# Kernel optimization log

Hardware: AMD Instinct MI355X
Metric: run time of the kernel (lower is better)

## Reference

```python
import jax, jax.numpy as jnp
import numpy as np

jax.config.update("jax_enable_x64", True)

B, S = 256, 256
TINY = float(np.finfo(np.float64).tiny)  # torch.finfo().tiny for double


def _matrix_tree_logZ(scores, mask):
    """scores: [B,S,S] float64, mask: [B,S] bool (col 0 is False).
    Returns sum over batch of log partition function (Matrix-Tree theorem)."""
    lens = mask.sum(-1)  # token counts per sentence (excludes root col)
    mask_r = mask.at[:, 0].set(True)  # index_fill(1, 0, 1)
    pair = mask_r[:, :, None] & mask_r[:, None, :]  # [B,S,S]
    s = jnp.where(pair, scores, -jnp.inf)
    m = jnp.max(s.reshape(s.shape[0], -1), axis=-1)  # [B] per-batch max for stability
    A = jnp.maximum(jnp.exp(s - m[:, None, None]), TINY)  # clamp like torch
    idx = jnp.arange(S)
    D = jnp.zeros_like(A).at[:, idx, idx].set(A.sum(-1))  # degree matrix
    eye = jnp.eye(S, dtype=A.dtype)
    # masked_scatter_: rows with mask_r True take (D - A) rows, else identity
    L = jnp.where(mask_r[:, :, None], D - A, eye)
    logZ = jnp.linalg.slogdet(L[:, 1:, 1:])[1] + m * lens
    return logZ.sum()


def setup_inputs() -> dict:
    key = jax.random.key(0)
    k1, k2 = jax.random.split(key)
    scores = jax.random.normal(k1, (B, S, S), dtype=jnp.float32)
    lens = jax.random.randint(k2, (B,), S // 2, S)  # sentence lengths
    pos = jnp.arange(S)
    # col 0 (pseudo root) False, padding beyond length False
    mask = (pos[None, :] >= 1) & (pos[None, :] < lens[:, None])
    return {"scores": scores, "mask": mask}


def reference(scores, mask):
    # mbr=True path: marginals = d logZ / d scores (computed in double like torch)
    s64 = scores.astype(jnp.float64)
    probs = jax.grad(_matrix_tree_logZ)(s64, mask)
    return probs.astype(jnp.float32)
```

## Files before the change

kernel.cpp:

```cpp
#include <hip/hip_runtime.h>
#include <math.h>


#define S 256
#define BB 256

__device__ __forceinline__ int rowmap(int lr, int kb) {
    int rt = lr >> 6;
    int rb = rt + (rt >= kb ? 1 : 0);
    return rb * 64 + (lr & 63);
}

__global__ __launch_bounds__(256) void k_max(const float* __restrict__ sc,
                                             float* __restrict__ partial) {
    int b = blockIdx.y, rg = blockIdx.x;
    const float4* p4 = (const float4*)(sc + (size_t)b * S * S + rg * 8192);
    int tid = threadIdx.x;
    float4 v[8];
    #pragma unroll
    for (int it = 0; it < 8; ++it) v[it] = p4[tid + 256 * it];
    float m = -1e30f;
    #pragma unroll
    for (int it = 0; it < 8; ++it)
        m = fmaxf(m, fmaxf(fmaxf(v[it].x, v[it].y), fmaxf(v[it].z, v[it].w)));
    for (int off = 32; off > 0; off >>= 1) m = fmaxf(m, __shfl_down(m, off));
    __shared__ float sm[4];
    if ((tid & 63) == 0) sm[tid >> 6] = m;
    __syncthreads();
    if (tid == 0) partial[b * 8 + rg] = fmaxf(fmaxf(sm[0], sm[1]), fmaxf(sm[2], sm[3]));
}

__global__ void k_n(const unsigned char* __restrict__ mk, const float* __restrict__ partial,
                    double* __restrict__ mb, int* __restrict__ nb) {
    int b = blockIdx.x, j = threadIdx.x;
    __shared__ int shc[4];

    const unsigned int* mw = (const unsigned int*)mk;
    unsigned int w0 = mw[0], w1 = mw[1];
    int mode = (w0 != 0u) ? 0 : ((w1 != 0u) ? 1 : 2);

    int c;
    if (mode == 0)      c = (mk[(size_t)b * S + j] != 0);
    else if (mode == 1) c = (((const int*)mk)[(size_t)b * S + j] != 0);
    else                c = (((const long long*)mk)[(size_t)b * S + j] != 0LL);

    int lane = j & 63, wid = j >> 6;
    int cs = c;
    for (int off = 32; off > 0; off >>= 1) cs += __shfl_down(cs, off);
    if (lane == 0) shc[wid] = cs;
    __syncthreads();
    if (j == 0) {
        nb[b] = shc[0] + shc[1] + shc[2] + shc[3];
        float mm = partial[b * 8];
        #pragma unroll
        for (int q = 1; q < 8; ++q) mm = fmaxf(mm, partial[b * 8 + q]);
        mb[b] = (double)mm;
    }
}

__global__ __launch_bounds__(256) void k_build(const float* __restrict__ sc,
                                               const double* __restrict__ mb,
                                               const int* __restrict__ nb,
                                               double* __restrict__ Mg) {
    int b = blockIdx.y;
    int wid = threadIdx.x >> 6, lane = threadIdx.x & 63;
    int p = blockIdx.x * 4 + wid;
    int n = nb[b];
    double m = mb[b];
    __shared__ double se[4][260];
    double* Mrow = Mg + ((size_t)b * S + p) * S;
    bool act = (p < n);
    double ssum = 0.0;
    #pragma unroll
    for (int c4 = 0; c4 < 4; ++c4) {
        int j = lane + 64 * c4;
        double ev = 0.0;
        if (act && j <= n)
            ev = (double)expf((float)((double)sc[((size_t)b * S + (p + 1)) * S + j] - m));
        se[wid][j] = ev;
        ssum += ev;
    }
    for (int off = 32; off > 0; off >>= 1) ssum += __shfl_down(ssum, off);
    ssum = __shfl(ssum, 0);
    __syncthreads();
    #pragma unroll
    for (int c4 = 0; c4 < 4; ++c4) {
        int j = lane + 64 * c4;
        double v;
        if (act && j < n) v = ((j == p) ? ssum : 0.0) - se[wid][j + 1];
        else              v = (j == p) ? 1.0 : 0.0;
        Mrow[j] = v;
    }
}

__global__ __launch_bounds__(512) void k_step(double* __restrict__ Mg, int kb) {
    int b = blockIdx.x;
    double* M = Mg + (size_t)b * S * S;
    int tid = threadIdx.x;
    __shared__ double H[64 * 256];
    __shared__ double SCR[3104];

    int i = tid >> 3, g = tid & 7, c0 = g << 3;
    double c[8];
    {
        const double* src = M + (size_t)(kb * 64 + i) * S + kb * 64 + c0;
        #pragma unroll
        for (int m2 = 0; m2 < 4; ++m2) {
            double2 t = *(const double2*)(src + 2 * m2);
            c[2 * m2] = t.x; c[2 * m2 + 1] = t.y;
        }
    }
    double* rbuf = SCR;
    double* cbuf = SCR + 128;
    if (i == 0) {
        #pragma unroll
        for (int u = 0; u < 8; ++u) rbuf[c0 + u] = c[u];
    }
    if (g == 0) cbuf[i] = c[0];
    for (int k = 0; k < 64; ++k) {
        int par = k & 1;
        __syncthreads();
        double pv = rbuf[par * 64 + k];
        double f  = cbuf[par * 64 + i];
        double rk[8];
        #pragma unroll
        for (int m2 = 0; m2 < 4; ++m2) {
            double2 t = *(const double2*)&rbuf[par * 64 + c0 + 2 * m2];
            rk[2 * m2] = t.x; rk[2 * m2 + 1] = t.y;
        }
        double pivinv = 1.0 / pv;
        int kg = k >> 3, ks = k & 7;
        if (i == k) {
            #pragma unroll
            for (int u = 0; u < 8; ++u)
                c[u] = ((g == kg) && (u == ks)) ? pivinv : c[u] * pivinv;
        } else {
            double gm = f * pivinv;
            #pragma unroll
            for (int u = 0; u < 8; ++u)
                c[u] = ((g == kg) && (u == ks)) ? (-gm) : fma(-gm, rk[u], c[u]);
        }
        int k1 = k + 1;
        if (k1 < 64) {
            if (i == k1) {
                #pragma unroll
                for (int u = 0; u < 8; ++u) rbuf[(par ^ 1) * 64 + c0 + u] = c[u];
            }
            if (g == (k1 >> 3)) cbuf[(par ^ 1) * 64 + i] = c[k1 & 7];
        }
    }
    __syncthreads();

    int tx = tid & 31, ty = tid >> 5;
    double* PT = SCR;
    double* Rc = SCR + 512;
    double2 ga[4][3];
    #pragma unroll
    for (int r = 0; r < 4; ++r)
        #pragma unroll
        for (int q = 0; q < 3; ++q) ga[r][q] = double2{0.0, 0.0};

    for (int cs = 0; cs < 8; ++cs) {
        if (g == cs) {
            #pragma unroll
            for (int u = 0; u < 8; ++u) PT[u * 64 + i] = c[u];
        }
        #pragma unroll
        for (int rep = 0; rep < 3; ++rep) {
            int idx = rep * 512 + tid;
            int sL = idx / 192, jj = idx - sL * 192;
            Rc[sL * 192 + jj] = M[(size_t)(kb * 64 + cs * 8 + sL) * S + rowmap(jj, kb)];
        }
        __syncthreads();
        #pragma unroll
        for (int sL = 0; sL < 8; ++sL) {
            double2 p01 = *(const double2*)&PT[sL * 64 + 4 * ty];
            double2 p23 = *(const double2*)&PT[sL * 64 + 4 * ty + 2];
            double2 r0 = *(const double2*)&Rc[sL * 192 + 2 * tx];
            double2 r1 = *(const double2*)&Rc[sL * 192 + 2 * tx + 64];
            double2 r2 = *(const double2*)&Rc[sL * 192 + 2 * tx + 128];
            ga[0][0].x = fma(p01.x, r0.x, ga[0][0].x); ga[0][0].y = fma(p01.x, r0.y, ga[0][0].y);
            ga[0][1].x = fma(p01.x, r1.x, ga[0][1].x); ga[0][1].y = fma(p01.x, r1.y, ga[0][1].y);
            ga[0][2].x = fma(p01.x, r2.x, ga[0][2].x); ga[0][2].y = fma(p01.x, r2.y, ga[0][2].y);
            ga[1][0].x = fma(p01.y, r0.x, ga[1][0].x); ga[1][0].y = fma(p01.y, r0.y, ga[1][0].y);
            ga[1][1].x = fma(p01.y, r1.x, ga[1][1].x); ga[1][1].y = fma(p01.y, r1.y, ga[1][1].y);
            ga[1][2].x = fma(p01.y, r2.x, ga[1][2].x); ga[1][2].y = fma(p01.y, r2.y, ga[1][2].y);
            ga[2][0].x = fma(p23.x, r0.x, ga[2][0].x); ga[2][0].y = fma(p23.x, r0.y, ga[2][0].y);
            ga[2][1].x = fma(p23.x, r1.x, ga[2][1].x); ga[2][1].y = fma(p23.x, r1.y, ga[2][1].y);
            ga[2][2].x = fma(p23.x, r2.x, ga[2][2].x); ga[2][2].y = fma(p23.x, r2.y, ga[2][2].y);
            ga[3][0].x = fma(p23.y, r0.x, ga[3][0].x); ga[3][0].y = fma(p23.y, r0.y, ga[3][0].y);
            ga[3][1].x = fma(p23.y, r1.x, ga[3][1].x); ga[3][1].y = fma(p23.y, r1.y, ga[3][1].y);
            ga[3][2].x = fma(p23.y, r2.x, ga[3][2].x); ga[3][2].y = fma(p23.y, r2.y, ga[3][2].y);
        }
        __syncthreads();
    }
    #pragma unroll
    for (int r = 0; r < 4; ++r)
        #pragma unroll
        for (int q = 0; q < 3; ++q) {
            int col = rowmap(2 * tx + 64 * q, kb);
            *(double2*)&H[(4 * ty + r) * 256 + col] = ga[r][q];
        }
    #pragma unroll
    for (int u = 0; u < 8; ++u) H[i * 256 + kb * 64 + c0 + u] = c[u];
    __syncthreads();

    #pragma unroll
    for (int rep = 0; rep < 16; ++rep) {
        int idx = rep * 512 + tid;
        int row = idx >> 7, col2 = idx & 127;
        *(double2*)&M[(size_t)(kb * 64 + row) * S + 2 * col2] =
            *(const double2*)&H[row * 256 + 2 * col2];
    }

    double* FT = SCR;
    for (int half = 0; half < 2; ++half) {
        double2 acc[6][4];
        #pragma unroll
        for (int q = 0; q < 6; ++q)
            #pragma unroll
            for (int w = 0; w < 4; ++w) acc[q][w] = double2{0.0, 0.0};

        for (int ck = 0; ck < 4; ++ck) {
            __syncthreads();
            #pragma unroll
            for (int rep = 0; rep < 3; ++rep) {
                int idx = rep * 512 + tid;
                int kk = idx & 15, lr = idx >> 4;
                FT[kk * 194 + lr] =
                    M[(size_t)rowmap(half * 96 + lr, kb) * S + kb * 64 + ck * 16 + kk];
            }
            __syncthreads();
            for (int kk = 0; kk < 16; ++kk) {
                int kr = ck * 16 + kk;
                double2 f01 = *(const double2*)&FT[kk * 194 + 6 * ty];
                double2 f23 = *(const double2*)&FT[kk * 194 + 6 * ty + 2];
                double2 f45 = *(const double2*)&FT[kk * 194 + 6 * ty + 4];
                #pragma unroll
                for (int w = 0; w < 4; ++w) {
                    double2 h = *(const double2*)&H[kr * 256 + 2 * tx + 64 * w];
                    acc[0][w].x = fma(f01.x, h.x, acc[0][w].x); acc[0][w].y = fma(f01.x, h.y, acc[0][w].y);
                    acc[1][w].x = fma(f01.y, h.x, acc[1][w].x); acc[1][w].y = fma(f01.y, h.y, acc[1][w].y);
                    acc[2][w].x = fma(f23.x, h.x, acc[2][w].x); acc[2][w].y = fma(f23.x, h.y, acc[2][w].y);
                    acc[3][w].x = fma(f23.y, h.x, acc[3][w].x); acc[3][w].y = fma(f23.y, h.y, acc[3][w].y);
                    acc[4][w].x = fma(f45.x, h.x, acc[4][w].x); acc[4][w].y = fma(f45.x, h.y, acc[4][w].y);
                    acc[5][w].x = fma(f45.y, h.x, acc[5][w].x); acc[5][w].y = fma(f45.y, h.y, acc[5][w].y);
                }
            }
        }
        #pragma unroll
        for (int q = 0; q < 6; ++q) {
            size_t row = (size_t)rowmap(half * 96 + 6 * ty + q, kb) * S;
            #pragma unroll
            for (int w = 0; w < 4; ++w) {
                int j0 = 2 * tx + 64 * w;
                if (w == kb) {
                    *(double2*)&M[row + j0] = double2{-acc[q][w].x, -acc[q][w].y};
                } else {
                    double2 old = *(const double2*)&M[row + j0];
                    *(double2*)&M[row + j0] = double2{old.x - acc[q][w].x, old.y - acc[q][w].y};
                }
            }
        }
    }
}

__global__ __launch_bounds__(256) void k_diag(const double* __restrict__ Mg,
                                              const float* __restrict__ sc,
                                              const double* __restrict__ mb,
                                              const int* __restrict__ nb,
                                              double* __restrict__ Dg,
                                              float* __restrict__ out) {
    int b = blockIdx.x, t = threadIdx.x;
    const double* M = Mg + (size_t)b * S * S;
    __shared__ double sd[256];
    double d = M[(size_t)t * S + t];
    sd[t] = d;
    Dg[(size_t)b * S + t] = d;
    out[(size_t)b * S * S + t] = 0.0f;
    __syncthreads();
    int n = nb[b];
    float m = (float)mb[b];
    if (t >= 1) {
        float v = 0.0f;
        if (t <= n) {
            double A = (double)expf(sc[((size_t)b * S + t) * S + 0] - m);
            v = (float)(A * sd[t - 1]);
        }
        out[((size_t)b * S + t) * S + 0] = v;
    }
}

__global__ __launch_bounds__(256) void k_xtepi(const double* __restrict__ Mg,
                                               const float* __restrict__ sc,
                                               const double* __restrict__ mb,
                                               const int* __restrict__ nb,
                                               const double* __restrict__ Dg,
                                               float* __restrict__ out) {
    int b = blockIdx.y, t = blockIdx.x;
    int r = t & 3, c = t >> 2;
    const double* M = Mg + (size_t)b * S * S;
    __shared__ float L[64][65];
    __shared__ double sdg[64];
    int tid = threadIdx.x;
    int cc = tid & 63;
    #pragma unroll
    for (int rep = 0; rep < 16; ++rep) {
        int rr = rep * 4 + (tid >> 6);
        L[rr][cc] = (float)M[(size_t)(64 * r + rr) * S + 64 * c + cc];
    }
    if (tid < 64) sdg[tid] = Dg[(size_t)b * S + 64 * c + tid];
    __syncthreads();
    int n = nb[b];
    float m = (float)mb[b];
    int pp = tid & 63;
    #pragma unroll
    for (int rep = 0; rep < 16; ++rep) {
        int qq = rep * 4 + (tid >> 6);
        int orow = 64 * c + qq + 1, ocol = 64 * r + pp + 1;
        if (orow < 256 && ocol < 256) {
            float v = 0.0f;
            if (orow <= n && ocol <= n) {
                double A = (double)expf(sc[((size_t)b * S + orow) * S + ocol] - m);
                v = (float)(A * (sdg[qq] - (double)L[pp][qq]));
            }
            out[((size_t)b * S + orow) * S + ocol] = v;
        }
    }
}

extern "C" void kernel_launch(void* const* d_in, const int* in_sizes, int n_in,
                              void* d_out, int out_size, void* d_ws, size_t ws_size,
                              hipStream_t stream) {
    (void)in_sizes; (void)n_in; (void)out_size; (void)ws_size;
    const float* sc = (const float*)d_in[0];
    const unsigned char* mk = (const unsigned char*)d_in[1];
    double* ws = (double*)d_ws;

    double* M  = ws;
    double* mb = M + (size_t)BB * S * S;
    int*    nb = (int*)(mb + BB);
    double* Dg = mb + 2 * BB;
    float*  partial = (float*)Dg;
    float*  out = (float*)d_out;

    k_max<<<dim3(8, BB), 256, 0, stream>>>(sc, partial);
    k_n<<<BB, 256, 0, stream>>>(mk, partial, mb, nb);
    k_build<<<dim3(64, BB), 256, 0, stream>>>(sc, mb, nb, M);
    for (int kb = 0; kb < 4; ++kb)
        k_step<<<BB, 512, 0, stream>>>(M, kb);
    k_diag<<<BB, 256, 0, stream>>>(M, sc, mb, nb, Dg, out);
    k_xtepi<<<dim3(16, BB), 256, 0, stream>>>(M, sc, mb, nb, Dg, out);
}
```

Measured before the change: 549.3 us.

## Use FP64 MFMA for trailing Schur-complement update in block elimination step

Replaces the scalar FMA register-tiled rank-64 update in k_step with MFMA f64 16x16x4 instructions. Each wave computes 16x32 output tiles, reading the pivot column directly from global memory, and discovers the MFMA output lane/row layout at runtime with a probe MFMA. A barrier orders the pivot-column writes after all reads. This aims to use matrix cores for the dominant FP64 GEMM work, at the cost of uncoalesced scalar global loads and stores and more barriers.

Result: slower. 579.6 us (+5.5%).

```diff
diff --git a/kernel.cpp b/kernel.cpp
--- a/kernel.cpp
+++ b/kernel.cpp
@@ -4,6 +4,8 @@
 
 #define S 256
 #define BB 256
+
+typedef double f64x4 __attribute__((ext_vector_type(4)));
 
 __device__ __forceinline__ int rowmap(int lr, int kb) {
     int rt = lr >> 6;
@@ -99,6 +101,24 @@
     int tid = threadIdx.x;
     __shared__ double H[64 * 256];
     __shared__ double SCR[3104];
+    __shared__ int rowtab[16];
+
+    int pl = tid & 63;
+    int pli = pl & 15, plk = pl >> 4;
+    {
+        f64x4 pr = {0.0, 0.0, 0.0, 0.0}, pc = {0.0, 0.0, 0.0, 0.0};
+        pr = __builtin_amdgcn_mfma_f64_16x16x4f64((plk == 0) ? (double)(pli + 1) : 0.0,
+                                                  (plk == 0 && pli == 0) ? 1.0 : 0.0,
+                                                  pr, 0, 0, 0);
+        pc = __builtin_amdgcn_mfma_f64_16x16x4f64((plk == 0) ? 1.0 : 0.0,
+                                                  (plk == 0) ? (double)(pli + 1) : 0.0,
+                                                  pc, 0, 0, 0);
+        int cof = (int)pc[0] - 1;
+        if (cof == 0) {
+            #pragma unroll
+            for (int v = 0; v < 4; ++v) rowtab[plk * 4 + v] = (int)pr[v] - 1;
+        }
+    }
 
     int i = tid >> 3, g = tid & 7, c0 = g << 3;
     double c[8];
@@ -213,53 +233,46 @@
             *(const double2*)&H[row * 256 + 2 * col2];
     }
 
-    double* FT = SCR;
-    for (int half = 0; half < 2; ++half) {
-        double2 acc[6][4];
-        #pragma unroll
-        for (int q = 0; q < 6; ++q)
-            #pragma unroll
-            for (int w = 0; w < 4; ++w) acc[q][w] = double2{0.0, 0.0};
-
-        for (int ck = 0; ck < 4; ++ck) {
+    {
+        int wv = tid >> 6;
+        int li = pli, lk = plk;
+        int ct0 = 2 * wv, ct1 = 2 * wv + 1;
+        bool pivw = ((wv >> 1) == kb);
+        f64x4 pc2 = {0.0, 0.0, 0.0, 0.0};
+        pc2 = __builtin_amdgcn_mfma_f64_16x16x4f64((lk == 0) ? 1.0 : 0.0,
+                                                   (lk == 0) ? (double)(li + 1) : 0.0,
+                                                   pc2, 0, 0, 0);
+        int cof = (int)pc2[0] - 1;
+        int r0 = rowtab[lk * 4 + 0], r1 = rowtab[lk * 4 + 1];
+        int r2 = rowtab[lk * 4 + 2], r3 = rowtab[lk * 4 + 3];
+        for (int rt = 0; rt < 12; ++rt) {
+            const double* Fp = M + (size_t)rowmap(rt * 16 + li, kb) * S + kb * 64 + lk;
+            f64x4 acc0 = {0.0, 0.0, 0.0, 0.0};
+            f64x4 acc1 = {0.0, 0.0, 0.0, 0.0};
+            #pragma unroll
+            for (int s = 0; s < 16; ++s) {
+                double a  = -Fp[4 * s];
+                double b0 = H[(4 * s + lk) * 256 + 16 * ct0 + li];
+                double b1 = H[(4 * s + lk) * 256 + 16 * ct1 + li];
+                acc0 = __builtin_amdgcn_mfma_f64_16x16x4f64(a, b0, acc0, 0, 0, 0);
+                acc1 = __builtin_amdgcn_mfma_f64_16x16x4f64(a, b1, acc1, 0, 0, 0);
+            }
+            size_t g0 = (size_t)rowmap(rt * 16 + r0, kb) * S;
+            size_t g1 = (size_t)rowmap(rt * 16 + r1, kb) * S;
+            size_t g2 = (size_t)rowmap(rt * 16 + r2, kb) * S;
+            size_t g3 = (size_t)rowmap(rt * 16 + r3, kb) * S;
+            if (!pivw) {
+                M[g0 + 16 * ct0 + cof] += acc0[0]; M[g0 + 16 * ct1 + cof] += acc1[0];
+                M[g1 + 16 * ct0 + cof] += acc0[1]; M[g1 + 16 * ct1 + cof] += acc1[1];
+                M[g2 + 16 * ct0 + cof] += acc0[2]; M[g2 + 16 * ct1 + cof] += acc1[2];
+                M[g3 + 16 * ct0 + cof] += acc0[3]; M[g3 + 16 * ct1 + cof] += acc1[3];
+            }
             __syncthreads();
-            #pragma unroll
-            for (int rep = 0; rep < 3; ++rep) {
-                int idx = rep * 512 + tid;
-                int kk = idx & 15, lr = idx >> 4;
-                FT[kk * 194 + lr] =
-                    M[(size_t)rowmap(half * 96 + lr, kb) * S + kb * 64 + ck * 16 + kk];
-            }
-            __syncthreads();
-            for (int kk = 0; kk < 16; ++kk) {
-                int kr = ck * 16 + kk;
-                double2 f01 = *(const double2*)&FT[kk * 194 + 6 * ty];
-                double2 f23 = *(const double2*)&FT[kk * 194 + 6 * ty + 2];
-                double2 f45 = *(const double2*)&FT[kk * 194 + 6 * ty + 4];
-                #pragma unroll
-                for (int w = 0; w < 4; ++w) {
-                    double2 h = *(const double2*)&H[kr * 256 + 2 * tx + 64 * w];
-                    acc[0][w].x = fma(f01.x, h.x, acc[0][w].x); acc[0][w].y = fma(f01.x, h.y, acc[0][w].y);
-                    acc[1][w].x = fma(f01.y, h.x, acc[1][w].x); acc[1][w].y = fma(f01.y, h.y, acc[1][w].y);
-                    acc[2][w].x = fma(f23.x, h.x, acc[2][w].x); acc[2][w].y = fma(f23.x, h.y, acc[2][w].y);
-                    acc[3][w].x = fma(f23.y, h.x, acc[3][w].x); acc[3][w].y = fma(f23.y, h.y, acc[3][w].y);
-                    acc[4][w].x = fma(f45.x, h.x, acc[4][w].x); acc[4][w].y = fma(f45.x, h.y, acc[4][w].y);
-                    acc[5][w].x = fma(f45.y, h.x, acc[5][w].x); acc[5][w].y = fma(f45.y, h.y, acc[5][w].y);
-                }
-            }
-        }
-        #pragma unroll
-        for (int q = 0; q < 6; ++q) {
-            size_t row = (size_t)rowmap(half * 96 + 6 * ty + q, kb) * S;
-            #pragma unroll
-            for (int w = 0; w < 4; ++w) {
-                int j0 = 2 * tx + 64 * w;
-                if (w == kb) {
-                    *(double2*)&M[row + j0] = double2{-acc[q][w].x, -acc[q][w].y};
-                } else {
-                    double2 old = *(const double2*)&M[row + j0];
-                    *(double2*)&M[row + j0] = double2{old.x - acc[q][w].x, old.y - acc[q][w].y};
-                }
+            if (pivw) {
+                M[g0 + 16 * ct0 + cof] = acc0[0]; M[g0 + 16 * ct1 + cof] = acc1[0];
+                M[g1 + 16 * ct0 + cof] = acc0[1]; M[g1 + 16 * ct1 + cof] = acc1[1];
+                M[g2 + 16 * ct0 + cof] = acc0[2]; M[g2 + 16 * ct1 + cof] = acc1[2];
+                M[g3 + 16 * ct0 + cof] = acc0[3]; M[g3 + 16 * ct1 + cof] = acc1[3];
             }
         }
     }
```
